# Kernel optimization log

Measured on AMD Instinct MI355X. Metric: run time of the kernel, lower is better.

The kernel has to match this reference:

```python
import jax, jax.numpy as jnp
import numpy as np

B, N, H = 32, 256, 1024
HEADS, NHID = 8, 128
NCLS = 7
BAND = 24
ALPHA = 0.2          # GAT leaky-relu slope
NEG = -9e15          # masked-attention fill, as in pyGAT


def setup_inputs() -> dict:
    key = jax.random.key(0)
    ks = jax.random.split(key, 16)
    def nrm(k, shp, s=0.02):
        return jax.random.normal(k, shp, dtype=jnp.float32) * s
    hidden_cls = jax.random.normal(ks[0], (B, N, H), dtype=jnp.float32)
    hidden_emo = jax.random.normal(ks[1], (B, N, H), dtype=jnp.float32)
    # causal band cliques, diagonal included (GAT uses clique - eye)
    t = jnp.arange(N)
    band = ((t[None, :] <= t[:, None]) & (t[None, :] > t[:, None] - BAND)).astype(jnp.float32)
    clique = jnp.broadcast_to(band, (B, N, N))
    labels = jax.random.randint(ks[2], (B, N), 0, NCLS)
    pooler_W = nrm(ks[3], (H, H)); pooler_b = jnp.zeros((H,), jnp.float32)
    gat_W = nrm(ks[4], (HEADS, H, NHID))
    gat_a1 = nrm(ks[5], (HEADS, NHID)); gat_a2 = nrm(ks[6], (HEADS, NHID))
    out_W = nrm(ks[7], (H, H))            # heads*nhid == H -> nclass=H
    out_a1 = nrm(ks[8], (H,)); out_a2 = nrm(ks[9], (H,))
    lin1_W = nrm(ks[10], (H, H)); lin1_b = jnp.zeros((H,), jnp.float32)
    lin0_W = nrm(ks[11], (2 * H, H)); lin0_b = jnp.zeros((H,), jnp.float32)
    cls_W = nrm(ks[12], (H, NCLS)); cls_b = jnp.zeros((NCLS,), jnp.float32)
    A = jax.random.uniform(ks[13], (NCLS, NCLS), dtype=jnp.float32) + 0.1
    hmm_A = A / A.sum(axis=1, keepdims=True)   # row-stochastic transition matrix
    return dict(hidden_cls=hidden_cls, hidden_emo=hidden_emo, clique=clique,
                labels=labels, pooler_W=pooler_W, pooler_b=pooler_b,
                gat_W=gat_W, gat_a1=gat_a1, gat_a2=gat_a2,
                out_W=out_W, out_a1=out_a1, out_a2=out_a2,
                lin1_W=lin1_W, lin1_b=lin1_b, lin0_W=lin0_W, lin0_b=lin0_b,
                cls_W=cls_W, cls_b=cls_b, hmm_A=hmm_A)


def _lrelu(x):
    return jnp.where(x > 0, x, ALPHA * x)


def reference(hidden_cls, hidden_emo, clique, labels, pooler_W, pooler_b,
              gat_W, gat_a1, gat_a2, out_W, out_a1, out_a2,
              lin1_W, lin1_b, lin0_W, lin0_b, cls_W, cls_b, hmm_A):
    # PoolerAll: dense + tanh on all token states (dropout = identity in eval)
    fea_cls = jnp.tanh(hidden_cls @ pooler_W + pooler_b)   # [B,N,H] (CLS per utt)
    fea_emo = jnp.tanh(hidden_emo @ pooler_W + pooler_b)   # [B,N,H] (mask tok per utt)

    eyeN = jnp.eye(N, dtype=clique.dtype)
    adjm = (clique - eyeN) > 0                             # [B,N,N] GAT adjacency

    def gat_one(x, am):                                    # x [N,H], am [N,N]
        Wh = jnp.einsum('nf,hfd->hnd', x, gat_W)           # [heads,N,nhid]
        e = _lrelu(jnp.einsum('hnd,hd->hn', Wh, gat_a1)[:, :, None]
                   + jnp.einsum('hnd,hd->hn', Wh, gat_a2)[:, None, :])
        att = jax.nn.softmax(jnp.where(am[None], e, NEG), axis=-1)
        h1 = jax.nn.elu(jnp.einsum('hnm,hmd->hnd', att, Wh))
        h1 = jnp.transpose(h1, (1, 0, 2)).reshape(N, HEADS * NHID)
        Wh2 = h1 @ out_W                                   # out attention layer (concat=False)
        e2 = _lrelu((Wh2 @ out_a1)[:, None] + (Wh2 @ out_a2)[None, :])
        h2 = jax.nn.softmax(jnp.where(am, e2, NEG), axis=-1) @ Wh2
        return jax.nn.elu(h2)                              # [N,H]

    gat_out = jax.vmap(gat_one)(fea_cls, adjm)             # [B,N,H]
    # row 0 replaced by (dropout of) fea_cls row 0, as in the original
    g = jnp.concatenate([fea_cls[:, :1], gat_out[:, 1:]], axis=1)
    g = jnp.concatenate([fea_cls, g @ lin1_W + lin1_b], axis=-1) @ lin0_W + lin0_b
    log_gat = jax.nn.softmax(g @ cls_W + cls_b, axis=-1)   # [B,N,NCLS] (probs)

    # HMM emission probs hmm_B(fea) = softmax(classifier(fea))
    Bprob = jax.nn.softmax(fea_emo @ cls_W + cls_b, axis=-1)  # [B,N,NCLS]
    P0 = jnp.full((NCLS,), 1.0 / NCLS, dtype=jnp.float32)
    AT = hmm_A.T

    def hmm_row(Bp, mrow):                                 # Bp [N,NCLS], mrow [N]
        def step(carry, xs):
            p, started = carry
            bt, m = xs
            p_init = P0 * bt; p_init = p_init / p_init.sum()
            p_tr = (AT @ p) * bt; p_tr = p_tr / p_tr.sum()
            p_new = jnp.where(started, p_tr, p_init)
            valid = m > 0.5
            return (jnp.where(valid, p_new, p), started | valid), None
        (p, _), _ = jax.lax.scan(step, (P0, jnp.asarray(False)), (Bp, mrow))
        return p                                           # final filtered posterior

    log_hmm = jax.vmap(lambda Bp, M: jax.vmap(lambda mr: hmm_row(Bp, mr))(M))(Bprob, clique)

    logits = jnp.log((log_gat + log_hmm) * 0.5).reshape(B * N, NCLS)
    lab = labels.reshape(B * N)
    mask = lab >= 0
    picked = jnp.take_along_axis(logits, jnp.where(mask, lab, 0)[:, None], axis=1)[:, 0]
    loss = -(jnp.where(mask, picked, 0.0).sum() / jnp.maximum(mask.sum(), 1).astype(jnp.float32))
    return loss, logits
```

## Files before the change

kernel.cpp:

```cpp
#include <hip/hip_runtime.h>
#include <hip/hip_bf16.h>
#include <math.h>

typedef __hip_bfloat16 bf16;
typedef __attribute__((ext_vector_type(8))) short short8;
typedef __attribute__((ext_vector_type(4))) float float4v;

static constexpr int Bb = 32, Nn = 256, Hh = 1024, HEADS = 8, NHID = 128, NCLS = 7, BAND = 24;
static constexpr int M = Bb * Nn;
static constexpr float ALPHA = 0.2f;
static constexpr long INEL = (long)M * Hh;

__device__ __forceinline__ float tof(bf16 x) { return __bfloat162float(x); }
__device__ __forceinline__ bf16 tob(float x) { return __float2bfloat16(x); }
__device__ __forceinline__ unsigned short f2bits(float x) {
    bf16 h = __float2bfloat16(x);
    return *(unsigned short*)&h;
}
__device__ __forceinline__ float bits2f(unsigned short u) {
    unsigned v = ((unsigned)u) << 16;
    float f;
    __builtin_memcpy(&f, &v, 4);
    return f;
}

__device__ __forceinline__ void gload16(const void* g, void* l) {
    __builtin_amdgcn_global_load_lds(
        (const __attribute__((address_space(1))) void*)g,
        (__attribute__((address_space(3))) void*)l, 16, 0, 0);
}

static constexpr long OFF_PWT  = 0;
static constexpr long OFF_PB   = 1048576;
static constexpr long OFF_WCT  = 1049600;
static constexpr long OFF_GA1  = 2098176;
static constexpr long OFF_GA2  = 2099200;
static constexpr long OFF_OWT  = 2100224;
static constexpr long OFF_OA1  = 3148800;
static constexpr long OFF_OA2  = 3149824;
static constexpr long OFF_L1WT = 3150848;
static constexpr long OFF_L1B  = 4199424;
static constexpr long OFF_L0WT = 4200448;
static constexpr long OFF_L0B  = 6297600;
static constexpr long OFF_CWT  = 6298624;
static constexpr long OFF_CB   = 6305792;
static constexpr long OFF_HA   = 6305799;
static constexpr long OFF_L1WN = 6305848;
static constexpr long W_TOTAL  = 7354424;
static constexpr long CONV_TOTAL = W_TOTAL + (2 * INEL) / 8;

__global__ void probe_k(const void* __restrict__ p, int* __restrict__ flag) {
    int t = threadIdx.x;
    int bad = 0;
    for (int i = t; i < 4096; i += 256) {
        float v = tof(((const bf16*)p)[i]);
        if (!(fabsf(v) < 1e4f)) bad = 1;
    }
    __shared__ int sb[256];
    sb[t] = bad; __syncthreads();
    for (int s = 128; s; s >>= 1) { if (t < s) sb[t] |= sb[t + s]; __syncthreads(); }
    if (t == 0) *flag = sb[0] ? 0 : 1;
}

__device__ __forceinline__ float ldany(const void* p, long i, int isb) {
    return isb ? tof(((const bf16*)p)[i]) : ((const float*)p)[i];
}

__global__ void convall_k(const int* __restrict__ flagp,
                          const void* pW, const void* pb, const void* gW,
                          const void* ga1, const void* ga2, const void* oW,
                          const void* oa1, const void* oa2, const void* l1W,
                          const void* l1b, const void* l0W, const void* l0b,
                          const void* cW, const void* cb, const void* hA,
                          const void* in0, const void* in1,
                          bf16* __restrict__ dst, bf16* __restrict__ din0,
                          bf16* __restrict__ din1) {
    long idx = (long)blockIdx.x * 256 + threadIdx.x;
    if (idx >= CONV_TOTAL) return;
    int isb = *flagp;
    if (idx >= W_TOTAL) {
        long g = (idx - W_TOTAL) * 8;
        const void* s; bf16* d; long off;
        if (g < INEL) { s = in0; d = din0; off = g; }
        else          { s = in1; d = din1; off = g - INEL; }
        if (isb) {
            *(int4*)(d + off) = *(const int4*)((const bf16*)s + off);
        } else {
            const float* f = (const float*)s + off;
            unsigned short tmp[8];
            #pragma unroll
            for (int q = 0; q < 8; ++q) tmp[q] = f2bits(f[q]);
            *(int4*)(d + off) = *(int4*)tmp;
        }
        return;
    }
    const void* src; long si;
    if      (idx < OFF_PB)   { long l = idx;            long n = l >> 10, k = l & 1023;
                               src = pW;  si = k * 1024 + n; }
    else if (idx < OFF_WCT)  { src = pb;  si = idx - OFF_PB; }
    else if (idx < OFF_GA1)  { long l = idx - OFF_WCT;  long n = l >> 10, f = l & 1023;
                               long h = n >> 7, d = n & 127;
                               src = gW;  si = h * 131072 + f * 128 + d; }
    else if (idx < OFF_GA2)  { src = ga1; si = idx - OFF_GA1; }
    else if (idx < OFF_OWT)  { src = ga2; si = idx - OFF_GA2; }
    else if (idx < OFF_OA1)  { long l = idx - OFF_OWT;  long n = l >> 10, k = l & 1023;
                               src = oW;  si = k * 1024 + n; }
    else if (idx < OFF_OA2)  { src = oa1; si = idx - OFF_OA1; }
    else if (idx < OFF_L1WT) { src = oa2; si = idx - OFF_OA2; }
    else if (idx < OFF_L1B)  { long l = idx - OFF_L1WT; long n = l >> 10, k = l & 1023;
                               src = l1W; si = k * 1024 + n; }
    else if (idx < OFF_L0WT) { src = l1b; si = idx - OFF_L1B; }
    else if (idx < OFF_L0B)  { long l = idx - OFF_L0WT; long n = l >> 11, k = l & 2047;
                               src = l0W; si = k * 1024 + n; }
    else if (idx < OFF_CWT)  { src = l0b; si = idx - OFF_L0B; }
    else if (idx < OFF_CB)   { long l = idx - OFF_CWT;  long c = l >> 10, k = l & 1023;
                               src = cW;  si = k * 7 + c; }
    else if (idx < OFF_HA)   { src = cb;  si = idx - OFF_CB; }
    else if (idx < OFF_L1WN) { src = hA;  si = idx - OFF_HA; }
    else                     { src = l1W; si = idx - OFF_L1WN; }
    dst[idx] = tob(ldany(src, si, isb));
}

__global__ void bias2_k(const bf16* __restrict__ wc, bf16* __restrict__ b2) {
    int n = blockIdx.x;
    int lane = threadIdx.x;
    const bf16* row = wc + OFF_L0WT + (long)n * 2048 + 1024;
    const bf16* l1b = wc + OFF_L1B;
    float s = 0.f;
    for (int j = lane; j < 1024; j += 64) s += tof(l1b[j]) * tof(row[j]);
    #pragma unroll
    for (int off = 32; off; off >>= 1) s += __shfl_down(s, off);
    if (lane == 0) b2[n] = tob(s + tof(wc[OFF_L0B + n]));
}

__device__ __forceinline__ void gemm_core(const bf16* __restrict__ A, int lda,
                                          const bf16* __restrict__ Bt, int ldb,
                                          const bf16* __restrict__ bias,
                                          bf16* __restrict__ Cout,
                                          unsigned short* As, unsigned short* Bs,
                                          int Nc, int K, int bm, int bn, int act) {
    const int tid = threadIdx.x;
    const int lane = tid & 63;
    const int wave = tid >> 6;
    const int wm = (wave >> 1) * 64, wn = (wave & 1) * 64;
    const int l15 = lane & 15, quad = lane >> 4;
    const int r0 = wave * 32;
    const int lrow = lane >> 2, q = lane & 3;
    const int rA = r0 + lrow, rB = r0 + 16 + lrow;
    const int qa = (q ^ (rA & 3) ^ ((rA >> 2) & 3)) * 8;
    const int qb = (q ^ (rB & 3) ^ ((rB >> 2) & 3)) * 8;
    const int sc8 = (quad ^ (l15 & 3) ^ (l15 >> 2)) * 8;

    float4v acc[4][4];
    #pragma unroll
    for (int i = 0; i < 4; ++i)
        #pragma unroll
        for (int j = 0; j < 4; ++j) acc[i][j] = (float4v){0.f, 0.f, 0.f, 0.f};

    const bf16* ga0 = A + (long)(bm + rA) * lda + qa;
    const bf16* ga1 = A + (long)(bm + rB) * lda + qb;
    const bf16* gb0 = Bt + (long)(bn + rA) * ldb + qa;
    const bf16* gb1 = Bt + (long)(bn + rB) * ldb + qb;

    for (int k0 = 0; k0 < K; k0 += 64) {
        gload16(ga0 + k0,      As + r0 * 32);
        gload16(ga1 + k0,      As + (r0 + 16) * 32);
        gload16(ga0 + k0 + 32, As + 4096 + r0 * 32);
        gload16(ga1 + k0 + 32, As + 4096 + (r0 + 16) * 32);
        gload16(gb0 + k0,      Bs + r0 * 32);
        gload16(gb1 + k0,      Bs + (r0 + 16) * 32);
        gload16(gb0 + k0 + 32, Bs + 4096 + r0 * 32);
        gload16(gb1 + k0 + 32, Bs + 4096 + (r0 + 16) * 32);
        __syncthreads();
        #pragma unroll
        for (int ks = 0; ks < 2; ++ks) {
            const unsigned short* Au = As + ks * 4096;
            const unsigned short* Bu = Bs + ks * 4096;
            short8 af[4], bfr[4];
            #pragma unroll
            for (int i = 0; i < 4; ++i)
                af[i] = *(const short8*)(Au + (wm + i * 16 + l15) * 32 + sc8);
            #pragma unroll
            for (int j = 0; j < 4; ++j)
                bfr[j] = *(const short8*)(Bu + (wn + j * 16 + l15) * 32 + sc8);
            #pragma unroll
            for (int i = 0; i < 4; ++i)
                #pragma unroll
                for (int j = 0; j < 4; ++j)
                    acc[i][j] = __builtin_amdgcn_mfma_f32_16x16x32_bf16(af[i], bfr[j], acc[i][j], 0, 0, 0);
        }
        __syncthreads();
    }
    #pragma unroll
    for (int j = 0; j < 4; ++j) {
        int gn = bn + wn + j * 16 + l15;
        float bj = bias ? tof(bias[gn]) : 0.f;
        #pragma unroll
        for (int i = 0; i < 4; ++i) {
            #pragma unroll
            for (int r = 0; r < 4; ++r) {
                int gm = bm + wm + i * 16 + quad * 4 + r;
                float v = acc[i][j][r] + bj;
                if (act == 1) v = tanhf(v);
                Cout[(long)gm * Nc + gn] = tob(v);
            }
        }
    }
}

__global__ __launch_bounds__(256) void gemm_fast_k(const bf16* __restrict__ A,
                                                   const bf16* __restrict__ Bt,
                                                   const bf16* __restrict__ bias,
                                                   bf16* __restrict__ Cout,
                                                   int Nc, int K) {
    __shared__ unsigned short As[2 * 128 * 32];
    __shared__ unsigned short Bs[2 * 128 * 32];
    gemm_core(A, K, Bt, K, bias, Cout, As, Bs, Nc, K, blockIdx.x * 128, blockIdx.y * 128, 0);
}

__global__ __launch_bounds__(256) void gemmP_k(const bf16* __restrict__ A0,
                                               const bf16* __restrict__ A1,
                                               const bf16* __restrict__ Bt,
                                               const bf16* __restrict__ bias,
                                               bf16* __restrict__ C0,
                                               bf16* __restrict__ C1,
                                               const bf16* __restrict__ wgA,
                                               const bf16* __restrict__ wgB,
                                               bf16* __restrict__ wgC) {
    __shared__ unsigned short As[2 * 128 * 32];
    __shared__ unsigned short Bs[2 * 128 * 32];
    const int z = blockIdx.z;
    if (z == 2) {
        if (blockIdx.x >= 8) return;
        gemm_core(wgA, 2048, wgB, 1024, (const bf16*)nullptr, wgC, As, Bs,
                  1024, 1024, blockIdx.x * 128, blockIdx.y * 128, 0);
    } else {
        gemm_core(z ? A1 : A0, 1024, Bt, 1024, bias, z ? C1 : C0, As, Bs,
                  1024, 1024, blockIdx.x * 128, blockIdx.y * 128, 1);
    }
}

__global__ __launch_bounds__(256) void gemm2_fast_k(const bf16* __restrict__ A1,
                                                    const bf16* __restrict__ B1,
                                                    const bf16* __restrict__ A2,
                                                    const bf16* __restrict__ B2,
                                                    const bf16* __restrict__ bias,
                                                    bf16* __restrict__ Cout) {
    constexpr int Nc = 1024;
    __shared__ unsigned short As[2 * 128 * 32];
    __shared__ unsigned short Bs[2 * 128 * 32];
    const int tid = threadIdx.x;
    const int lane = tid & 63;
    const int wave = tid >> 6;
    const int wm = (wave >> 1) * 64, wn = (wave & 1) * 64;
    const int l15 = lane & 15, quad = lane >> 4;
    const int r0 = wave * 32;
    const int lrow = lane >> 2, q = lane & 3;
    const int rA = r0 + lrow, rB = r0 + 16 + lrow;
    const int qa = (q ^ (rA & 3) ^ ((rA >> 2) & 3)) * 8;
    const int qb = (q ^ (rB & 3) ^ ((rB >> 2) & 3)) * 8;
    const int sc8 = (quad ^ (l15 & 3) ^ (l15 >> 2)) * 8;
    const int bm = blockIdx.x * 128, bn = blockIdx.y * 128;

    float4v acc[4][4];
    #pragma unroll
    for (int i = 0; i < 4; ++i)
        #pragma unroll
        for (int j = 0; j < 4; ++j) acc[i][j] = (float4v){0.f, 0.f, 0.f, 0.f};

    for (int k0 = 0; k0 < 2048; k0 += 64) {
        const int sel = (k0 < 1024);
        const bf16* Asrc = sel ? A1 : A2;
        const bf16* Bsrc = sel ? B1 : B2;
        const int ldb = sel ? 2048 : 1024;
        const int kl = k0 & 1023;
        const bf16* ga0 = Asrc + (long)(bm + rA) * 1024 + kl + qa;
        const bf16* ga1 = Asrc + (long)(bm + rB) * 1024 + kl + qb;
        const bf16* gb0 = Bsrc + (long)(bn + rA) * ldb + kl + qa;
        const bf16* gb1 = Bsrc + (long)(bn + rB) * ldb + kl + qb;
        gload16(ga0,      As + r0 * 32);
        gload16(ga1,      As + (r0 + 16) * 32);
        gload16(ga0 + 32, As + 4096 + r0 * 32);
        gload16(ga1 + 32, As + 4096 + (r0 + 16) * 32);
        gload16(gb0,      Bs + r0 * 32);
        gload16(gb1,      Bs + (r0 + 16) * 32);
        gload16(gb0 + 32, Bs + 4096 + r0 * 32);
        gload16(gb1 + 32, Bs + 4096 + (r0 + 16) * 32);
        __syncthreads();
        #pragma unroll
        for (int ks = 0; ks < 2; ++ks) {
            const unsigned short* Au = As + ks * 4096;
            const unsigned short* Bu = Bs + ks * 4096;
            short8 af[4], bfr[4];
            #pragma unroll
            for (int i = 0; i < 4; ++i)
                af[i] = *(const short8*)(Au + (wm + i * 16 + l15) * 32 + sc8);
            #pragma unroll
            for (int j = 0; j < 4; ++j)
                bfr[j] = *(const short8*)(Bu + (wn + j * 16 + l15) * 32 + sc8);
            #pragma unroll
            for (int i = 0; i < 4; ++i)
                #pragma unroll
                for (int j = 0; j < 4; ++j)
                    acc[i][j] = __builtin_amdgcn_mfma_f32_16x16x32_bf16(af[i], bfr[j], acc[i][j], 0, 0, 0);
        }
        __syncthreads();
    }
    #pragma unroll
    for (int j = 0; j < 4; ++j) {
        int gn = bn + wn + j * 16 + l15;
        float bj = tof(bias[gn]);
        #pragma unroll
        for (int i = 0; i < 4; ++i)
            #pragma unroll
            for (int r = 0; r < 4; ++r) {
                int gm = bm + wm + i * 16 + quad * 4 + r;
                Cout[(long)gm * Nc + gn] = tob(acc[i][j][r] + bj);
            }
    }
}

__global__ __launch_bounds__(256) void att1f_k(const bf16* __restrict__ Wh,
                                               const bf16* __restrict__ ga1,
                                               const bf16* __restrict__ ga2,
                                               bf16* __restrict__ h1) {
    __shared__ unsigned short S[152][128];
    __shared__ float f1s[152], f2s[152];
    __shared__ float att[128][25];
    const int bx = blockIdx.x;
    const int b = bx >> 4, h = (bx >> 1) & 7, half = bx & 1;
    const int nbase = half * 128;
    const int mstart = half ? (nbase - (BAND - 1)) : 0;
    const int mcount = half ? (256 - mstart) : 128;
    const int t = threadIdx.x;
    const int c = t & 15;

    float av1[8], av2[8];
    {
        union { int4 v; unsigned short us[8]; } u1, u2;
        u1.v = *(const int4*)(ga1 + h * 128 + c * 8);
        u2.v = *(const int4*)(ga2 + h * 128 + c * 8);
        #pragma unroll
        for (int qq = 0; qq < 8; ++qq) { av1[qq] = bits2f(u1.us[qq]); av2[qq] = bits2f(u2.us[qq]); }
    }

    const int iters = (mcount * 16 + 255) >> 8;
    for (int i = 0; i < iters; ++i) {
        int li = i * 256 + t;
        int mr = li >> 4;
        if (mr < mcount) {
            long ga = (long)(b * 256 + mstart + mr) * 1024 + h * 128 + c * 8;
            union { int4 v; unsigned short us[8]; } u;
            u.v = *(const int4*)(Wh + ga);
            float p1 = 0.f, p2 = 0.f;
            #pragma unroll
            for (int qq = 0; qq < 8; ++qq) {
                float f = bits2f(u.us[qq]);
                p1 += f * av1[qq]; p2 += f * av2[qq];
            }
            *(int4*)&S[mr][c * 8] = u.v;
            #pragma unroll
            for (int mask = 1; mask < 16; mask <<= 1) {
                p1 += __shfl_xor(p1, mask);
                p2 += __shfl_xor(p2, mask);
            }
            if (c == 0) { f1s[mr] = p1; f2s[mr] = p2; }
        }
    }
    __syncthreads();

    if (t < 128) {
        int n = nbase + t;
        if (n > 0) {
            int cnt = n < (BAND - 1) ? n : (BAND - 1);
            int m0 = n - cnt;
            float f1n = f1s[n - mstart];
            float e[BAND - 1];
            float mx = -1e30f;
            for (int i = 0; i < cnt; ++i) {
                float v = f1n + f2s[m0 + i - mstart];
                v = v > 0.f ? v : ALPHA * v;
                e[i] = v; mx = fmaxf(mx, v);
            }
            float ss = 0.f;
            for (int i = 0; i < cnt; ++i) { e[i] = __expf(e[i] - mx); ss += e[i]; }
            float inv = 1.0f / ss;
            for (int i = 0; i < cnt; ++i) att[t][i] = e[i] * inv;
        }
    }
    __syncthreads();

    const int wave = t >> 6, lane = t & 63;
    for (int ln = wave; ln < 128; ln += 4) {
        int n = nbase + ln;
        if (n == 0) continue;
        int cnt = n < (BAND - 1) ? n : (BAND - 1);
        int mr0 = n - cnt - mstart;
        float s0 = 0.f, s1 = 0.f;
        for (int i = 0; i < cnt; ++i) {
            float a = att[ln][i];
            unsigned u = *(const unsigned*)&S[mr0 + i][lane * 2];
            s0 += a * bits2f((unsigned short)(u & 0xffff));
            s1 += a * bits2f((unsigned short)(u >> 16));
        }
        s0 = s0 > 0.f ? s0 : expm1f(s0);
        s1 = s1 > 0.f ? s1 : expm1f(s1);
        unsigned out = (unsigned)f2bits(s0) | ((unsigned)f2bits(s1) << 16);
        *(unsigned*)(h1 + (long)(b * 256 + n) * 1024 + h * 128 + lane * 2) = out;
    }
}

__global__ void mean1_k(const bf16* __restrict__ Wh, bf16* __restrict__ h1) {
    int bh = blockIdx.x;
    int h = bh & 7, b = bh >> 3;
    int lane = threadIdx.x;
    float s0 = 0.f, s1 = 0.f;
    long base = (long)(b * 256) * 1024 + h * 128 + lane * 2;
    for (int m = 0; m < 256; ++m) {
        unsigned u = *(const unsigned*)(Wh + base + (long)m * 1024);
        s0 += bits2f((unsigned short)(u & 0xffff));
        s1 += bits2f((unsigned short)(u >> 16));
    }
    s0 *= (1.0f / 256.0f); s1 *= (1.0f / 256.0f);
    s0 = s0 > 0.f ? s0 : expm1f(s0);
    s1 = s1 > 0.f ? s1 : expm1f(s1);
    unsigned out = (unsigned)f2bits(s0) | ((unsigned)f2bits(s1) << 16);
    *(unsigned*)(h1 + base) = out;
}

__global__ void f12b_k(const bf16* __restrict__ Wh2, const bf16* __restrict__ a1,
                       const bf16* __restrict__ a2, float* __restrict__ f1b,
                       float* __restrict__ f2b) {
    int idx = blockIdx.x;
    int lane = threadIdx.x;
    const bf16* row = Wh2 + (long)idx * 1024 + lane * 16;
    float s1 = 0.f, s2 = 0.f;
    #pragma unroll
    for (int half = 0; half < 2; ++half) {
        union { int4 v; unsigned short us[8]; } x, w1, w2;
        x.v  = *(const int4*)(row + half * 8);
        w1.v = *(const int4*)(a1 + lane * 16 + half * 8);
        w2.v = *(const int4*)(a2 + lane * 16 + half * 8);
        #pragma unroll
        for (int q = 0; q < 8; ++q) {
            float f = bits2f(x.us[q]);
            s1 += f * bits2f(w1.us[q]);
            s2 += f * bits2f(w2.us[q]);
        }
    }
    #pragma unroll
    for (int off = 32; off; off >>= 1) {
        s1 += __shfl_down(s1, off);
        s2 += __shfl_down(s2, off);
    }
    if (lane == 0) { f1b[idx] = s1; f2b[idx] = s2; }
}

__global__ __launch_bounds__(256) void att2f_k(const bf16* __restrict__ Wh2,
                                               const float* __restrict__ f1b,
                                               const float* __restrict__ f2b,
                                               const bf16* __restrict__ fea_cls,
                                               bf16* __restrict__ g) {
    __shared__ unsigned short S[152][128];
    __shared__ float att[128][25];
    const int bx = blockIdx.x;
    const int b = bx >> 4, half = (bx >> 3) & 1, jt = bx & 7;
    const int nbase = half * 128;
    const int mstart = half ? (nbase - (BAND - 1)) : 0;
    const int mcount = half ? (256 - mstart) : 128;
    const int t = threadIdx.x;
    const int c = t & 15;

    if (half == 0 && t < 16) {
        long base = (long)(b * 256) * 1024 + jt * 128 + t * 8;
        *(int4*)(g + base) = *(const int4*)(fea_cls + base);
    }

    const int iters = (mcount * 16 + 255) >> 8;
    for (int i = 0; i < iters; ++i) {
        int li = i * 256 + t;
        int mr = li >> 4;
        if (mr < mcount) {
            long ga = (long)(b * 256 + mstart + mr) * 1024 + jt * 128 + c * 8;
            *(int4*)&S[mr][c * 8] = *(const int4*)(Wh2 + ga);
        }
    }
    __syncthreads();

    if (t < 128) {
        int n = nbase + t;
        if (n > 0) {
            int cnt = n < (BAND - 1) ? n : (BAND - 1);
            int m0 = n - cnt;
            float f1n = f1b[b * 256 + n];
            float e[BAND - 1];
            float mx = -1e30f;
            for (int i = 0; i < cnt; ++i) {
                float v = f1n + f2b[b * 256 + m0 + i];
                v = v > 0.f ? v : ALPHA * v;
                e[i] = v; mx = fmaxf(mx, v);
            }
            float ss = 0.f;
            for (int i = 0; i < cnt; ++i) { e[i] = __expf(e[i] - mx); ss += e[i]; }
            float inv = 1.0f / ss;
            for (int i = 0; i < cnt; ++i) att[t][i] = e[i] * inv;
        }
    }
    __syncthreads();

    const int wave = t >> 6, lane = t & 63;
    for (int ln = wave; ln < 128; ln += 4) {
        int n = nbase + ln;
        if (n == 0) continue;
        int cnt = n < (BAND - 1) ? n : (BAND - 1);
        int mr0 = n - cnt - mstart;
        float s0 = 0.f, s1 = 0.f;
        for (int i = 0; i < cnt; ++i) {
            float a = att[ln][i];
            unsigned u = *(const unsigned*)&S[mr0 + i][lane * 2];
            s0 += a * bits2f((unsigned short)(u & 0xffff));
            s1 += a * bits2f((unsigned short)(u >> 16));
        }
        s0 = s0 > 0.f ? s0 : expm1f(s0);
        s1 = s1 > 0.f ? s1 : expm1f(s1);
        unsigned out = (unsigned)f2bits(s0) | ((unsigned)f2bits(s1) << 16);
        *(unsigned*)(g + (long)(b * 256 + n) * 1024 + jt * 128 + lane * 2) = out;
    }
}

__global__ void cls7_k(const bf16* __restrict__ X, const bf16* __restrict__ Wt,
                       const bf16* __restrict__ b, float* __restrict__ out, int K) {
    int row = blockIdx.x;
    int lane = threadIdx.x;
    float xv[16];
    {
        const bf16* x = X + (long)row * K + lane * 16;
        union { int4 v; unsigned short us[8]; } u0, u1;
        u0.v = *(const int4*)x; u1.v = *(const int4*)(x + 8);
        #pragma unroll
        for (int q = 0; q < 8; ++q) { xv[q] = bits2f(u0.us[q]); xv[q + 8] = bits2f(u1.us[q]); }
    }
    float acc[NCLS];
    #pragma unroll
    for (int cc = 0; cc < NCLS; ++cc) {
        const bf16* wr = Wt + (long)cc * K + lane * 16;
        union { int4 v; unsigned short us[8]; } w0, w1;
        w0.v = *(const int4*)wr; w1.v = *(const int4*)(wr + 8);
        float s = 0.f;
        #pragma unroll
        for (int q = 0; q < 8; ++q) {
            s += xv[q] * bits2f(w0.us[q]);
            s += xv[q + 8] * bits2f(w1.us[q]);
        }
        acc[cc] = s;
    }
    #pragma unroll
    for (int cc = 0; cc < NCLS; ++cc)
        #pragma unroll
        for (int off = 32; off; off >>= 1) acc[cc] += __shfl_down(acc[cc], off);
    if (lane == 0) {
        float mx = -1e30f;
        #pragma unroll
        for (int cc = 0; cc < NCLS; ++cc) { acc[cc] += tof(b[cc]); mx = fmaxf(mx, acc[cc]); }
        float s = 0.f;
        #pragma unroll
        for (int cc = 0; cc < NCLS; ++cc) { acc[cc] = expf(acc[cc] - mx); s += acc[cc]; }
        float inv = 1.0f / s;
        #pragma unroll
        for (int cc = 0; cc < NCLS; ++cc) out[(long)row * NCLS + cc] = acc[cc] * inv;
    }
}

__global__ void zero_k(float* p) { *p = 0.f; }

__global__ void final_k(const float* __restrict__ lg, const float* __restrict__ Bprob,
                        const bf16* __restrict__ hmm_A, const int* __restrict__ labels,
                        void* __restrict__ out, float* __restrict__ loss_acc,
                        const int* __restrict__ flagp) {
    __shared__ float AT[NCLS][NCLS];
    int t = threadIdx.x;
    if (t < NCLS * NCLS) AT[t / NCLS][t % NCLS] = tof(hmm_A[(t % NCLS) * NCLS + t / NCLS]);
    __syncthreads();
    int idx = blockIdx.x * 256 + t;
    int n = idx & 255, b = idx >> 8;
    int t0 = n - (BAND - 1) > 0 ? n - (BAND - 1) : 0;
    const float* Bp = Bprob + (long)(b * 256) * NCLS;
    float p[NCLS];
    {
        float s = 0.f;
        #pragma unroll
        for (int cc = 0; cc < NCLS; ++cc) { p[cc] = Bp[t0 * NCLS + cc]; s += p[cc]; }
        float inv = 1.0f / s;
        #pragma unroll
        for (int cc = 0; cc < NCLS; ++cc) p[cc] *= inv;
        for (int tt = t0 + 1; tt <= n; ++tt) {
            float qv[NCLS]; float ss = 0.f;
            #pragma unroll
            for (int i = 0; i < NCLS; ++i) {
                float a = 0.f;
                #pragma unroll
                for (int j = 0; j < NCLS; ++j) a += AT[i][j] * p[j];
                a *= Bp[tt * NCLS + i];
                qv[i] = a; ss += a;
            }
            float iv = 1.0f / ss;
            #pragma unroll
            for (int i = 0; i < NCLS; ++i) p[i] = qv[i] * iv;
        }
    }
    const int isb = *flagp;
    int lab = labels[idx];
    float lo[NCLS];
    #pragma unroll
    for (int c = 0; c < NCLS; ++c) {
        float v = logf(0.5f * (lg[(long)idx * NCLS + c] + p[c]));
        lo[c] = v;
        long o = 1 + (long)idx * NCLS + c;
        if (isb) ((bf16*)out)[o] = tob(v);
        else     ((float*)out)[o] = v;
    }
    float picked = lo[lab];
    __shared__ float red[256];
    red[t] = picked;
    __syncthreads();
    for (int s = 128; s; s >>= 1) {
        if (t < s) red[t] += red[t + s];
        __syncthreads();
    }
    if (t == 0) atomicAdd(loss_acc, red[0]);
}

__global__ void loss_k(const float* __restrict__ acc, void* __restrict__ out,
                       const int* __restrict__ flagp) {
    float v = -acc[0] / (float)(Bb * Nn);
    if (*flagp) ((bf16*)out)[0] = tob(v);
    else        ((float*)out)[0] = v;
}

extern "C" void kernel_launch(void* const* d_in, const int* in_sizes, int n_in,
                              void* d_out, int out_size, void* d_ws, size_t ws_size,
                              hipStream_t stream) {
    const void* hidden_cls = d_in[0];
    const void* hidden_emo = d_in[1];
    const int* labels = (const int*)d_in[3];

    char* w = (char*)d_ws;
    bf16* C  = (bf16*)w;
    bf16* E  = C + INEL;
    bf16* Wb = E + INEL;
    bf16* H2 = Wb + INEL;
    bf16* wc = H2 + INEL;
    bf16* WgT = wc + W_TOTAL;
    bf16* b2  = WgT + (long)Hh * Hh;
    float* f1b   = (float*)(b2 + Hh);
    float* f2b   = f1b + M;
    float* Bprob = f2b + M;
    float* lgat  = Bprob + (long)M * NCLS;
    float* loss_acc = lgat + (long)M * NCLS;
    int*   flag  = (int*)(loss_acc + 1);

    dim3 gblk(256);
    dim3 ggrid(M / 128, Hh / 128);
    dim3 pgrid(M / 128, Hh / 128, 3);

    probe_k<<<1, 256, 0, stream>>>(d_in[4], flag);
    convall_k<<<(int)((CONV_TOTAL + 255) / 256), 256, 0, stream>>>(
        flag, d_in[4], d_in[5], d_in[6], d_in[7], d_in[8], d_in[9], d_in[10],
        d_in[11], d_in[12], d_in[13], d_in[14], d_in[15], d_in[16], d_in[17],
        d_in[18], hidden_emo, hidden_cls, wc, Wb, H2);
    bias2_k<<<Hh, 64, 0, stream>>>(wc, b2);

    gemmP_k<<<pgrid, gblk, 0, stream>>>(Wb, H2, wc + OFF_PWT, wc + OFF_PB, E, C,
                                        wc + OFF_L0WT + 1024, wc + OFF_L1WN, WgT);
    cls7_k<<<M, 64, 0, stream>>>(E, wc + OFF_CWT, wc + OFF_CB, Bprob, Hh);
    gemm_fast_k<<<ggrid, gblk, 0, stream>>>(C, wc + OFF_WCT, (const bf16*)nullptr, Wb, Hh, Hh);
    att1f_k<<<512, 256, 0, stream>>>(Wb, wc + OFF_GA1, wc + OFF_GA2, E);
    mean1_k<<<Bb * HEADS, 64, 0, stream>>>(Wb, E);
    gemm_fast_k<<<ggrid, gblk, 0, stream>>>(E, wc + OFF_OWT, (const bf16*)nullptr, Wb, Hh, Hh);
    f12b_k<<<M, 64, 0, stream>>>(Wb, wc + OFF_OA1, wc + OFF_OA2, f1b, f2b);
    att2f_k<<<512, 256, 0, stream>>>(Wb, f1b, f2b, C, E);
    gemm2_fast_k<<<ggrid, gblk, 0, stream>>>(C, wc + OFF_L0WT, E, WgT, b2, Wb);
    cls7_k<<<M, 64, 0, stream>>>(Wb, wc + OFF_CWT, wc + OFF_CB, lgat, Hh);
    zero_k<<<1, 1, 0, stream>>>(loss_acc);
    final_k<<<M / 256, 256, 0, stream>>>(lgat, Bprob, wc + OFF_HA, labels, d_out, loss_acc, flag);
    loss_k<<<1, 1, 0, stream>>>(loss_acc, d_out, flag);
}
```

Measured before the change: 489.9 us.

## Drop LDS staging in GEMMs and load MFMA fragments directly from global memory

Replaces the LDS-staged tile loads (global_load_lds plus barriers) in the shared GEMM core and the dual-source GEMM with per-lane direct 16-byte global loads feeding the MFMA operands. This removes the LDS round trip and the two block barriers per k-step. In exchange, each wave fetches its own fragments, so data is no longer shared through LDS across waves. That increases global/L2 traffic fourfold-ish and relies on cache hits, and the loads are uncoalesced strided row reads.

```diff
diff --git a/kernel.cpp b/kernel.cpp
--- a/kernel.cpp
+++ b/kernel.cpp
@@ -22,12 +22,6 @@
     float f;
     __builtin_memcpy(&f, &v, 4);
     return f;
-}
-
-__device__ __forceinline__ void gload16(const void* g, void* l) {
-    __builtin_amdgcn_global_load_lds(
-        (const __attribute__((address_space(1))) void*)g,
-        (__attribute__((address_space(3))) void*)l, 16, 0, 0);
 }
 
 static constexpr long OFF_PWT  = 0;
@@ -137,19 +131,12 @@
                                           const bf16* __restrict__ Bt, int ldb,
                                           const bf16* __restrict__ bias,
                                           bf16* __restrict__ Cout,
-                                          unsigned short* As, unsigned short* Bs,
                                           int Nc, int K, int bm, int bn, int act) {
     const int tid = threadIdx.x;
     const int lane = tid & 63;
     const int wave = tid >> 6;
     const int wm = (wave >> 1) * 64, wn = (wave & 1) * 64;
     const int l15 = lane & 15, quad = lane >> 4;
-    const int r0 = wave * 32;
-    const int lrow = lane >> 2, q = lane & 3;
-    const int rA = r0 + lrow, rB = r0 + 16 + lrow;
-    const int qa = (q ^ (rA & 3) ^ ((rA >> 2) & 3)) * 8;
-    const int qb = (q ^ (rB & 3) ^ ((rB >> 2) & 3)) * 8;
-    const int sc8 = (quad ^ (l15 & 3) ^ (l15 >> 2)) * 8;
 
     float4v acc[4][4];
     #pragma unroll
@@ -157,39 +144,25 @@
         #pragma unroll
         for (int j = 0; j < 4; ++j) acc[i][j] = (float4v){0.f, 0.f, 0.f, 0.f};
 
-    const bf16* ga0 = A + (long)(bm + rA) * lda + qa;
-    const bf16* ga1 = A + (long)(bm + rB) * lda + qb;
-    const bf16* gb0 = Bt + (long)(bn + rA) * ldb + qa;
-    const bf16* gb1 = Bt + (long)(bn + rB) * ldb + qb;
-
-    for (int k0 = 0; k0 < K; k0 += 64) {
-        gload16(ga0 + k0,      As + r0 * 32);
-        gload16(ga1 + k0,      As + (r0 + 16) * 32);
-        gload16(ga0 + k0 + 32, As + 4096 + r0 * 32);
-        gload16(ga1 + k0 + 32, As + 4096 + (r0 + 16) * 32);
-        gload16(gb0 + k0,      Bs + r0 * 32);
-        gload16(gb1 + k0,      Bs + (r0 + 16) * 32);
-        gload16(gb0 + k0 + 32, Bs + 4096 + r0 * 32);
-        gload16(gb1 + k0 + 32, Bs + 4096 + (r0 + 16) * 32);
-        __syncthreads();
-        #pragma unroll
-        for (int ks = 0; ks < 2; ++ks) {
-            const unsigned short* Au = As + ks * 4096;
-            const unsigned short* Bu = Bs + ks * 4096;
-            short8 af[4], bfr[4];
-            #pragma unroll
-            for (int i = 0; i < 4; ++i)
-                af[i] = *(const short8*)(Au + (wm + i * 16 + l15) * 32 + sc8);
+    const bf16* pa[4];
+    const bf16* pb[4];
+    #pragma unroll
+    for (int i = 0; i < 4; ++i) pa[i] = A + (long)(bm + wm + i * 16 + l15) * lda + quad * 8;
+    #pragma unroll
+    for (int j = 0; j < 4; ++j) pb[j] = Bt + (long)(bn + wn + j * 16 + l15) * ldb + quad * 8;
+
+    #pragma unroll 2
+    for (int k0 = 0; k0 < K; k0 += 32) {
+        short8 af[4], bfr[4];
+        #pragma unroll
+        for (int i = 0; i < 4; ++i) af[i] = *(const short8*)(pa[i] + k0);
+        #pragma unroll
+        for (int j = 0; j < 4; ++j) bfr[j] = *(const short8*)(pb[j] + k0);
+        #pragma unroll
+        for (int i = 0; i < 4; ++i)
             #pragma unroll
             for (int j = 0; j < 4; ++j)
-                bfr[j] = *(const short8*)(Bu + (wn + j * 16 + l15) * 32 + sc8);
-            #pragma unroll
-            for (int i = 0; i < 4; ++i)
-                #pragma unroll
-                for (int j = 0; j < 4; ++j)
-                    acc[i][j] = __builtin_amdgcn_mfma_f32_16x16x32_bf16(af[i], bfr[j], acc[i][j], 0, 0, 0);
-        }
-        __syncthreads();
+                acc[i][j] = __builtin_amdgcn_mfma_f32_16x16x32_bf16(af[i], bfr[j], acc[i][j], 0, 0, 0);
     }
     #pragma unroll
     for (int j = 0; j < 4; ++j) {
@@ -213,9 +186,7 @@
                                                    const bf16* __restrict__ bias,
                                                    bf16* __restrict__ Cout,
                                                    int Nc, int K) {
-    __shared__ unsigned short As[2 * 128 * 32];
-    __shared__ unsigned short Bs[2 * 128 * 32];
-    gemm_core(A, K, Bt, K, bias, Cout, As, Bs, Nc, K, blockIdx.x * 128, blockIdx.y * 128, 0);
+    gemm_core(A, K, Bt, K, bias, Cout, Nc, K, blockIdx.x * 128, blockIdx.y * 128, 0);
 }
 
 __global__ __launch_bounds__(256) void gemmP_k(const bf16* __restrict__ A0,
@@ -227,15 +198,13 @@
                                                const bf16* __restrict__ wgA,
                                                const bf16* __restrict__ wgB,
                                                bf16* __restrict__ wgC) {
-    __shared__ unsigned short As[2 * 128 * 32];
-    __shared__ unsigned short Bs[2 * 128 * 32];
     const int z = blockIdx.z;
     if (z == 2) {
         if (blockIdx.x >= 8) return;
-        gemm_core(wgA, 2048, wgB, 1024, (const bf16*)nullptr, wgC, As, Bs,
+        gemm_core(wgA, 2048, wgB, 1024, (const bf16*)nullptr, wgC,
                   1024, 1024, blockIdx.x * 128, blockIdx.y * 128, 0);
     } else {
-        gemm_core(z ? A1 : A0, 1024, Bt, 1024, bias, z ? C1 : C0, As, Bs,
+        gemm_core(z ? A1 : A0, 1024, Bt, 1024, bias, z ? C1 : C0,
                   1024, 1024, blockIdx.x * 128, blockIdx.y * 128, 1);
     }
 }
@@ -247,19 +216,11 @@
                                                     const bf16* __restrict__ bias,
                                                     bf16* __restrict__ Cout) {
     constexpr int Nc = 1024;
-    __shared__ unsigned short As[2 * 128 * 32];
-    __shared__ unsigned short Bs[2 * 128 * 32];
     const int tid = threadIdx.x;
     const int lane = tid & 63;
     const int wave = tid >> 6;
     const int wm = (wave >> 1) * 64, wn = (wave & 1) * 64;
     const int l15 = lane & 15, quad = lane >> 4;
-    const int r0 = wave * 32;
-    const int lrow = lane >> 2, q = lane & 3;
-    const int rA = r0 + lrow, rB = r0 + 16 + lrow;
-    const int qa = (q ^ (rA & 3) ^ ((rA >> 2) & 3)) * 8;
-    const int qb = (q ^ (rB & 3) ^ ((rB >> 2) & 3)) * 8;
-    const int sc8 = (quad ^ (l15 & 3) ^ (l15 >> 2)) * 8;
     const int bm = blockIdx.x * 128, bn = blockIdx.y * 128;
 
     float4v acc[4][4];
@@ -268,43 +229,30 @@
         #pragma unroll
         for (int j = 0; j < 4; ++j) acc[i][j] = (float4v){0.f, 0.f, 0.f, 0.f};
 
-    for (int k0 = 0; k0 < 2048; k0 += 64) {
-        const int sel = (k0 < 1024);
-        const bf16* Asrc = sel ? A1 : A2;
-        const bf16* Bsrc = sel ? B1 : B2;
-        const int ldb = sel ? 2048 : 1024;
-        const int kl = k0 & 1023;
-        const bf16* ga0 = Asrc + (long)(bm + rA) * 1024 + kl + qa;
-        const bf16* ga1 = Asrc + (long)(bm + rB) * 1024 + kl + qb;
-        const bf16* gb0 = Bsrc + (long)(bn + rA) * ldb + kl + qa;
-        const bf16* gb1 = Bsrc + (long)(bn + rB) * ldb + kl + qb;
-        gload16(ga0,      As + r0 * 32);
-        gload16(ga1,      As + (r0 + 16) * 32);
-        gload16(ga0 + 32, As + 4096 + r0 * 32);
-        gload16(ga1 + 32, As + 4096 + (r0 + 16) * 32);
-        gload16(gb0,      Bs + r0 * 32);
-        gload16(gb1,      Bs + (r0 + 16) * 32);
-        gload16(gb0 + 32, Bs + 4096 + r0 * 32);
-        gload16(gb1 + 32, Bs + 4096 + (r0 + 16) * 32);
-        __syncthreads();
-        #pragma unroll
-        for (int ks = 0; ks < 2; ++ks) {
-            const unsigned short* Au = As + ks * 4096;
-            const unsigned short* Bu = Bs + ks * 4096;
+    #pragma unroll
+    for (int half = 0; half < 2; ++half) {
+        const bf16* Asrc = half ? A2 : A1;
+        const bf16* Bsrc = half ? B2 : B1;
+        const int ldb = half ? 1024 : 2048;
+        const bf16* pa[4];
+        const bf16* pb[4];
+        #pragma unroll
+        for (int i = 0; i < 4; ++i) pa[i] = Asrc + (long)(bm + wm + i * 16 + l15) * 1024 + quad * 8;
+        #pragma unroll
+        for (int j = 0; j < 4; ++j) pb[j] = Bsrc + (long)(bn + wn + j * 16 + l15) * ldb + quad * 8;
+        #pragma unroll 2
+        for (int k0 = 0; k0 < 1024; k0 += 32) {
             short8 af[4], bfr[4];
             #pragma unroll
-            for (int i = 0; i < 4; ++i)
-                af[i] = *(const short8*)(Au + (wm + i * 16 + l15) * 32 + sc8);
-            #pragma unroll
-            for (int j = 0; j < 4; ++j)
-                bfr[j] = *(const short8*)(Bu + (wn + j * 16 + l15) * 32 + sc8);
+            for (int i = 0; i < 4; ++i) af[i] = *(const short8*)(pa[i] + k0);
+            #pragma unroll
+            for (int j = 0; j < 4; ++j) bfr[j] = *(const short8*)(pb[j] + k0);
             #pragma unroll
             for (int i = 0; i < 4; ++i)
                 #pragma unroll
                 for (int j = 0; j < 4; ++j)
                     acc[i][j] = __builtin_amdgcn_mfma_f32_16x16x32_bf16(af[i], bfr[j], acc[i][j], 0, 0, 0);
         }
-        __syncthreads();
     }
     #pragma unroll
     for (int j = 0; j < 4; ++j) {
```

Result: slower. 718.9 us (+46.8%).
